# Optimization experiments

Hardware: AMD Instinct MI355X
Metric: run time of the kernel (lower is better)

Reference implementation:

```python
import jax, jax.numpy as jnp
import numpy as np

H, W, C = 768, 768, 64


def _segment_ids(mask):
    """mask: [L] int binary separator mask -> [L] int32 segment ids.
    A new grid segment starts at each rising edge (0 -> 1) of the mask;
    pixel 0 always belongs to segment 0. Equivalent to GridStructureBuilder's
    run-based row/column partition, derived via a single cumsum."""
    m = mask.astype(jnp.int32)
    prev = jnp.concatenate([jnp.zeros((1,), jnp.int32), m[:-1]])
    rising = ((m == 1) & (prev == 0)).at[0].set(False)
    return jnp.cumsum(rising.astype(jnp.int32))


def setup_inputs() -> dict:
    key = jax.random.key(0)
    k1, k2, k3 = jax.random.split(key, 3)
    return {
        "input": jax.random.normal(k1, (1, H, W, C), dtype=jnp.float32),
        "h_mask": jax.random.randint(k2, (1, H), 0, 2, dtype=jnp.int32),
        "v_mask": jax.random.randint(k3, (1, W), 0, 2, dtype=jnp.int32),
    }


def reference(input, h_mask, v_mask):
    x = input[0]                      # [H, W, C]
    h, w, c = x.shape
    row_ids = _segment_ids(h_mask[0])  # [H]
    col_ids = _segment_ids(v_mask[0])  # [W]
    # flat cell id per pixel; w is a static upper bound on the column count
    idx = (row_ids[:, None] * w + col_ids[None, :]).reshape(-1)  # [H*W]
    xf = x.reshape(h * w, c)
    n_seg = h * w                      # static upper bound on cell count
    sums = jax.ops.segment_sum(xf, idx, num_segments=n_seg)           # [n_seg, C]
    counts = jax.ops.segment_sum(jnp.ones((h * w,), x.dtype), idx,
                                 num_segments=n_seg)                  # [n_seg]
    # scatter-add of (1/area)*x == per-cell mean
    means = sums / jnp.maximum(counts, 1.0)[:, None]
    # keep_size=True: gather cell means back to every pixel
    return means[idx].reshape(1, h, w, c)
```

## Files before the change

kernel.cpp:

```cpp
#include <hip/hip_runtime.h>


#define GH 768
#define GW 768
#define GC 64
#define MAXSEG 385

enum {
    OFF_ROWSTART = 0,
    OFF_ROWEND   = OFF_ROWSTART + MAXSEG,
    OFF_COLSTART = OFF_ROWEND + MAXSEG,
    OFF_COLEND   = OFF_COLSTART + MAXSEG,
    OFF_NROWS    = OFF_COLEND + MAXSEG,
    OFF_NCOLS    = OFF_NROWS + 1,
};

__global__ __launch_bounds__(768) void seg_scan(const int* __restrict__ h_mask,
                                                const int* __restrict__ v_mask,
                                                int* __restrict__ ws) {
    __shared__ int s[GH];
    const int i = threadIdx.x;
    const bool is_row = (blockIdx.x == 0);
    const int* m = is_row ? h_mask : v_mask;

    int mi = m[i];
    int rising = 0;
    if (i > 0) rising = (mi == 1 && m[i - 1] == 0) ? 1 : 0;
    s[i] = rising;
    __syncthreads();

    for (int off = 1; off < GH; off <<= 1) {
        int add = (i >= off) ? s[i - off] : 0;
        __syncthreads();
        s[i] += add;
        __syncthreads();
    }

    const int seg  = s[i];
    const int segL = (i == 0)      ? -1 : s[i - 1];
    const int segR = (i == GH - 1) ? -2 : s[i + 1];

    int* start = ws + (is_row ? OFF_ROWSTART : OFF_COLSTART);
    int* end   = ws + (is_row ? OFF_ROWEND   : OFF_COLEND);
    if (seg != segL) start[seg] = i;
    if (seg != segR) end[seg]   = i + 1;
    if (i == GH - 1) ws[is_row ? OFF_NROWS : OFF_NCOLS] = seg + 1;
}

__global__ __launch_bounds__(256) void cell_pool(const float4* __restrict__ in,
                                                 float4* __restrict__ out,
                                                 const int* __restrict__ ws) {
    const int nrows  = ws[OFF_NROWS];
    const int ncols  = ws[OFF_NCOLS];
    const int ncells = nrows * ncols;

    const int wave   = blockIdx.x * 4 + (threadIdx.x >> 6);
    const int nwaves = gridDim.x * 4;
    const int lane   = threadIdx.x & 63;
    const int pg     = lane >> 4;
    const int cq     = lane & 15;

    for (int cell = wave; cell < ncells; cell += nwaves) {
        const int br = cell / ncols;
        const int bc = cell - br * ncols;
        const int y0 = ws[OFF_ROWSTART + br];
        const int y1 = ws[OFF_ROWEND + br];
        const int x0 = ws[OFF_COLSTART + bc];
        const int x1 = ws[OFF_COLEND + bc];

        float4 acc = make_float4(0.f, 0.f, 0.f, 0.f);
        for (int y = y0; y < y1; ++y) {
            const size_t rb = (size_t)(y * GW) * 16 + cq;
            for (int x = x0 + pg; x < x1; x += 4) {
                float4 v = in[rb + (size_t)x * 16];
                acc.x += v.x; acc.y += v.y; acc.z += v.z; acc.w += v.w;
            }
        }
        #pragma unroll
        for (int msk = 16; msk < 64; msk <<= 1) {
            acc.x += __shfl_xor(acc.x, msk, 64);
            acc.y += __shfl_xor(acc.y, msk, 64);
            acc.z += __shfl_xor(acc.z, msk, 64);
            acc.w += __shfl_xor(acc.w, msk, 64);
        }
        const float area = (float)((y1 - y0) * (x1 - x0));
        float4 mean;
        mean.x = acc.x / area; mean.y = acc.y / area;
        mean.z = acc.z / area; mean.w = acc.w / area;

        for (int y = y0; y < y1; ++y) {
            const size_t rb = (size_t)(y * GW) * 16 + cq;
            for (int x = x0 + pg; x < x1; x += 4) {
                out[rb + (size_t)x * 16] = mean;
            }
        }
    }
}

extern "C" void kernel_launch(void* const* d_in, const int* in_sizes, int n_in,
                              void* d_out, int out_size, void* d_ws, size_t ws_size,
                              hipStream_t stream) {
    const float* in  = (const float*)d_in[0];
    const int* hmask = (const int*)d_in[1];
    const int* vmask = (const int*)d_in[2];
    float* out = (float*)d_out;
    int* ws = (int*)d_ws;

    seg_scan<<<2, GH, 0, stream>>>(hmask, vmask, ws);
    cell_pool<<<2048, 256, 0, stream>>>((const float4*)in, (float4*)out, ws);
}
```

Before: 282.0 us.

## Use atomic work queue and flattened pixel loop for narrow cells

Replaces static round-robin cell assignment with a global atomic counter that hands out two cells at a time to each wave, which balances the uneven cell sizes across waves. Cells narrower than four columns now iterate over flattened pixel indices so all four pixel groups in the wave stay busy. The wide-cell loop uses two accumulators to expose more independent loads. The cost is an atomic on every dequeue, plus the queue head must be reset inside seg_scan on every launch.

```diff
diff --git a/kernel.cpp b/kernel.cpp
--- a/kernel.cpp
+++ b/kernel.cpp
@@ -3,7 +3,6 @@
 
 #define GH 768
 #define GW 768
-#define GC 64
 #define MAXSEG 385
 
 enum {
@@ -13,7 +12,12 @@
     OFF_COLEND   = OFF_COLSTART + MAXSEG,
     OFF_NROWS    = OFF_COLEND + MAXSEG,
     OFF_NCOLS    = OFF_NROWS + 1,
+    OFF_QHEAD    = OFF_NCOLS + 1,
 };
+
+__device__ __forceinline__ void acc4(float4& a, const float4 v) {
+    a.x += v.x; a.y += v.y; a.z += v.z; a.w += v.w;
+}
 
 __global__ __launch_bounds__(768) void seg_scan(const int* __restrict__ h_mask,
                                                 const int* __restrict__ v_mask,
@@ -45,53 +49,91 @@
     if (seg != segL) start[seg] = i;
     if (seg != segR) end[seg]   = i + 1;
     if (i == GH - 1) ws[is_row ? OFF_NROWS : OFF_NCOLS] = seg + 1;
+    if (i == 0 && is_row) ws[OFF_QHEAD] = 0;
 }
 
 __global__ __launch_bounds__(256) void cell_pool(const float4* __restrict__ in,
                                                  float4* __restrict__ out,
-                                                 const int* __restrict__ ws) {
+                                                 int* __restrict__ ws) {
     const int nrows  = ws[OFF_NROWS];
     const int ncols  = ws[OFF_NCOLS];
     const int ncells = nrows * ncols;
 
-    const int wave   = blockIdx.x * 4 + (threadIdx.x >> 6);
-    const int nwaves = gridDim.x * 4;
-    const int lane   = threadIdx.x & 63;
-    const int pg     = lane >> 4;
-    const int cq     = lane & 15;
+    const int lane = threadIdx.x & 63;
+    const int pg   = lane >> 4;
+    const int cq   = lane & 15;
 
-    for (int cell = wave; cell < ncells; cell += nwaves) {
-        const int br = cell / ncols;
-        const int bc = cell - br * ncols;
-        const int y0 = ws[OFF_ROWSTART + br];
-        const int y1 = ws[OFF_ROWEND + br];
-        const int x0 = ws[OFF_COLSTART + bc];
-        const int x1 = ws[OFF_COLEND + bc];
+    for (;;) {
+        int c0 = 0;
+        if (lane == 0) c0 = atomicAdd(ws + OFF_QHEAD, 2);
+        c0 = __shfl(c0, 0, 64);
+        if (c0 >= ncells) break;
+        const int cend = (c0 + 2 < ncells) ? c0 + 2 : ncells;
 
-        float4 acc = make_float4(0.f, 0.f, 0.f, 0.f);
-        for (int y = y0; y < y1; ++y) {
-            const size_t rb = (size_t)(y * GW) * 16 + cq;
-            for (int x = x0 + pg; x < x1; x += 4) {
-                float4 v = in[rb + (size_t)x * 16];
-                acc.x += v.x; acc.y += v.y; acc.z += v.z; acc.w += v.w;
+        for (int cell = c0; cell < cend; ++cell) {
+            const int br = cell / ncols;
+            const int bc = cell - br * ncols;
+            const int y0 = ws[OFF_ROWSTART + br];
+            const int y1 = ws[OFF_ROWEND + br];
+            const int x0 = ws[OFF_COLSTART + bc];
+            const int x1 = ws[OFF_COLEND + bc];
+            const int h   = y1 - y0;
+            const int wdt = x1 - x0;
+            const int npx = h * wdt;
+
+            float4 a0 = make_float4(0.f, 0.f, 0.f, 0.f);
+            float4 a1 = make_float4(0.f, 0.f, 0.f, 0.f);
+
+            if (wdt >= 4) {
+                for (int y = y0; y < y1; ++y) {
+                    const size_t rb = (size_t)(y * GW) * 16 + cq;
+                    int x = x0 + pg;
+                    for (; x + 4 < x1; x += 8) {
+                        float4 v0 = in[rb + (size_t)x * 16];
+                        float4 v1 = in[rb + (size_t)(x + 4) * 16];
+                        acc4(a0, v0);
+                        acc4(a1, v1);
+                    }
+                    for (; x < x1; x += 4) acc4(a0, in[rb + (size_t)x * 16]);
+                }
+            } else {
+                for (int base = 0; base < npx; base += 4) {
+                    const int p = base + pg;
+                    if (p < npx) {
+                        const int yy = p / wdt;
+                        const int xx = p - yy * wdt;
+                        acc4(a0, in[((size_t)((y0 + yy) * GW + x0 + xx)) * 16 + cq]);
+                    }
+                }
             }
-        }
-        #pragma unroll
-        for (int msk = 16; msk < 64; msk <<= 1) {
-            acc.x += __shfl_xor(acc.x, msk, 64);
-            acc.y += __shfl_xor(acc.y, msk, 64);
-            acc.z += __shfl_xor(acc.z, msk, 64);
-            acc.w += __shfl_xor(acc.w, msk, 64);
-        }
-        const float area = (float)((y1 - y0) * (x1 - x0));
-        float4 mean;
-        mean.x = acc.x / area; mean.y = acc.y / area;
-        mean.z = acc.z / area; mean.w = acc.w / area;
+            acc4(a0, a1);
+            #pragma unroll
+            for (int msk = 16; msk < 64; msk <<= 1) {
+                a0.x += __shfl_xor(a0.x, msk, 64);
+                a0.y += __shfl_xor(a0.y, msk, 64);
+                a0.z += __shfl_xor(a0.z, msk, 64);
+                a0.w += __shfl_xor(a0.w, msk, 64);
+            }
+            const float area = (float)npx;
+            float4 mean;
+            mean.x = a0.x / area; mean.y = a0.y / area;
+            mean.z = a0.z / area; mean.w = a0.w / area;
 
-        for (int y = y0; y < y1; ++y) {
-            const size_t rb = (size_t)(y * GW) * 16 + cq;
-            for (int x = x0 + pg; x < x1; x += 4) {
-                out[rb + (size_t)x * 16] = mean;
+            if (wdt >= 4) {
+                for (int y = y0; y < y1; ++y) {
+                    const size_t rb = (size_t)(y * GW) * 16 + cq;
+                    for (int x = x0 + pg; x < x1; x += 4)
+                        out[rb + (size_t)x * 16] = mean;
+                }
+            } else {
+                for (int base = 0; base < npx; base += 4) {
+                    const int p = base + pg;
+                    if (p < npx) {
+                        const int yy = p / wdt;
+                        const int xx = p - yy * wdt;
+                        out[((size_t)((y0 + yy) * GW + x0 + xx)) * 16 + cq] = mean;
+                    }
+                }
             }
         }
     }
```

Measured after the change: 529.0 us. +87.6%, slower.

## Split cell pooling into separable column-sum, cell-mean, and broadcast kernels

Applied to the files above, without the earlier changes.

Replaces the one-wave-per-cell pooling kernel with three kernels. The first reduces each row segment into per-column partial sums, using the output buffer as scratch. The second sums those partials over each column segment to get cell means in the workspace, and the third broadcasts the means to every pixel with fully coalesced writes. This aims to fix the poor load balance and strided small-cell access of the per-cell loop. It costs two extra launches plus the intermediate traffic, and it only runs when the workspace is large enough, otherwise falling back to the old kernel.

```diff
diff --git a/kernel.cpp b/kernel.cpp
--- a/kernel.cpp
+++ b/kernel.cpp
@@ -3,8 +3,8 @@
 
 #define GH 768
 #define GW 768
-#define GC 64
 #define MAXSEG 385
+#define ROWQ (GW * 16)
 
 enum {
     OFF_ROWSTART = 0,
@@ -13,7 +13,16 @@
     OFF_COLEND   = OFF_COLSTART + MAXSEG,
     OFF_NROWS    = OFF_COLEND + MAXSEG,
     OFF_NCOLS    = OFF_NROWS + 1,
+    OFF_RID      = OFF_NCOLS + 3,
+    OFF_CID      = OFF_RID + GH,
+    OFF_END      = OFF_CID + GW,
 };
+#define MEAN_OFF_BYTES 16384
+#define MEAN_CAP_BYTES ((size_t)MAXSEG * MAXSEG * 64 * 4)
+
+__device__ __forceinline__ void acc4(float4& a, const float4 v) {
+    a.x += v.x; a.y += v.y; a.z += v.z; a.w += v.w;
+}
 
 __global__ __launch_bounds__(768) void seg_scan(const int* __restrict__ h_mask,
                                                 const int* __restrict__ v_mask,
@@ -44,7 +53,69 @@
     int* end   = ws + (is_row ? OFF_ROWEND   : OFF_COLEND);
     if (seg != segL) start[seg] = i;
     if (seg != segR) end[seg]   = i + 1;
+    ws[(is_row ? OFF_RID : OFF_CID) + i] = seg;
     if (i == GH - 1) ws[is_row ? OFF_NROWS : OFF_NCOLS] = seg + 1;
+}
+
+__global__ __launch_bounds__(256) void col_sum(const float4* __restrict__ in,
+                                               float4* __restrict__ colsum,
+                                               const int* __restrict__ ws) {
+    const int N = ws[OFF_NROWS] * ROWQ;
+    const int stride = gridDim.x * blockDim.x;
+    for (int u = blockIdx.x * blockDim.x + threadIdx.x; u < N; u += stride) {
+        const int r   = u / ROWQ;
+        const int rem = u - r * ROWQ;
+        const int y0 = ws[OFF_ROWSTART + r];
+        const int y1 = ws[OFF_ROWEND + r];
+        float4 a0 = make_float4(0.f, 0.f, 0.f, 0.f);
+        float4 a1 = make_float4(0.f, 0.f, 0.f, 0.f);
+        int y = y0;
+        for (; y + 1 < y1; y += 2) {
+            acc4(a0, in[(size_t)y * ROWQ + rem]);
+            acc4(a1, in[(size_t)(y + 1) * ROWQ + rem]);
+        }
+        if (y < y1) acc4(a0, in[(size_t)y * ROWQ + rem]);
+        acc4(a0, a1);
+        colsum[u] = a0;
+    }
+}
+
+__global__ __launch_bounds__(256) void cell_mean(const float4* __restrict__ colsum,
+                                                 float4* __restrict__ mean,
+                                                 const int* __restrict__ ws) {
+    const int nrows = ws[OFF_NROWS];
+    const int ncols = ws[OFF_NCOLS];
+    const int N = nrows * ncols * 16;
+    const int stride = gridDim.x * blockDim.x;
+    for (int v = blockIdx.x * blockDim.x + threadIdx.x; v < N; v += stride) {
+        const int cq = v & 15;
+        const int rs = v >> 4;
+        const int r  = rs / ncols;
+        const int s  = rs - r * ncols;
+        const int x0 = ws[OFF_COLSTART + s];
+        const int x1 = ws[OFF_COLEND + s];
+        float4 a = make_float4(0.f, 0.f, 0.f, 0.f);
+        for (int x = x0; x < x1; ++x)
+            acc4(a, colsum[(size_t)r * ROWQ + x * 16 + cq]);
+        const float area =
+            (float)((ws[OFF_ROWEND + r] - ws[OFF_ROWSTART + r]) * (x1 - x0));
+        float4 mn;
+        mn.x = a.x / area; mn.y = a.y / area; mn.z = a.z / area; mn.w = a.w / area;
+        mean[v] = mn;
+    }
+}
+
+__global__ __launch_bounds__(256) void bcast(const float4* __restrict__ mean,
+                                             float4* __restrict__ out,
+                                             const int* __restrict__ ws) {
+    const int y  = blockIdx.y;
+    const int id = blockIdx.x * 256 + threadIdx.x;
+    const int x  = id >> 4;
+    const int cq = id & 15;
+    const int rid = ws[OFF_RID + y];
+    const int cid = ws[OFF_CID + x];
+    const int ncols = ws[OFF_NCOLS];
+    out[(size_t)y * ROWQ + id] = mean[((size_t)rid * ncols + cid) * 16 + cq];
 }
 
 __global__ __launch_bounds__(256) void cell_pool(const float4* __restrict__ in,
@@ -68,31 +139,26 @@
         const int x0 = ws[OFF_COLSTART + bc];
         const int x1 = ws[OFF_COLEND + bc];
 
-        float4 acc = make_float4(0.f, 0.f, 0.f, 0.f);
+        float4 a = make_float4(0.f, 0.f, 0.f, 0.f);
         for (int y = y0; y < y1; ++y) {
-            const size_t rb = (size_t)(y * GW) * 16 + cq;
-            for (int x = x0 + pg; x < x1; x += 4) {
-                float4 v = in[rb + (size_t)x * 16];
-                acc.x += v.x; acc.y += v.y; acc.z += v.z; acc.w += v.w;
-            }
+            const size_t rb = (size_t)y * ROWQ + cq;
+            for (int x = x0 + pg; x < x1; x += 4)
+                acc4(a, in[rb + (size_t)x * 16]);
         }
         #pragma unroll
         for (int msk = 16; msk < 64; msk <<= 1) {
-            acc.x += __shfl_xor(acc.x, msk, 64);
-            acc.y += __shfl_xor(acc.y, msk, 64);
-            acc.z += __shfl_xor(acc.z, msk, 64);
-            acc.w += __shfl_xor(acc.w, msk, 64);
+            a.x += __shfl_xor(a.x, msk, 64);
+            a.y += __shfl_xor(a.y, msk, 64);
+            a.z += __shfl_xor(a.z, msk, 64);
+            a.w += __shfl_xor(a.w, msk, 64);
         }
         const float area = (float)((y1 - y0) * (x1 - x0));
-        float4 mean;
-        mean.x = acc.x / area; mean.y = acc.y / area;
-        mean.z = acc.z / area; mean.w = acc.w / area;
-
+        float4 mn;
+        mn.x = a.x / area; mn.y = a.y / area; mn.z = a.z / area; mn.w = a.w / area;
         for (int y = y0; y < y1; ++y) {
-            const size_t rb = (size_t)(y * GW) * 16 + cq;
-            for (int x = x0 + pg; x < x1; x += 4) {
-                out[rb + (size_t)x * 16] = mean;
-            }
+            const size_t rb = (size_t)y * ROWQ + cq;
+            for (int x = x0 + pg; x < x1; x += 4)
+                out[rb + (size_t)x * 16] = mn;
         }
     }
 }
@@ -107,5 +173,15 @@
     int* ws = (int*)d_ws;
 
     seg_scan<<<2, GH, 0, stream>>>(hmask, vmask, ws);
-    cell_pool<<<2048, 256, 0, stream>>>((const float4*)in, (float4*)out, ws);
+
+    if (ws_size >= MEAN_OFF_BYTES + MEAN_CAP_BYTES) {
+        float4* colsum = (float4*)d_out;
+        float4* mean   = (float4*)((char*)d_ws + MEAN_OFF_BYTES);
+        col_sum<<<4096, 256, 0, stream>>>((const float4*)in, colsum, ws);
+        cell_mean<<<2048, 256, 0, stream>>>(colsum, mean, ws);
+        dim3 cgrid(GW * 16 / 256, GH);
+        bcast<<<cgrid, 256, 0, stream>>>(mean, (float4*)out, ws);
+    } else {
+        cell_pool<<<2048, 256, 0, stream>>>((const float4*)in, (float4*)out, ws);
+    }
 }
```

Measured after the change: 291.1 us. 1.03x slower.

## Pool cells via row-strip column tiles with shared-memory column sums

Applied to the files above, without the earlier changes.

Adds a strip_pool kernel in which each block handles one row segment across a tile of up to 64 columns built from whole column segments. Column sums go to shared memory and per-cell means are derived from them, so loads and stores are wide and coalesced instead of one wave walking tiny cells. The scan kernel now packs column segments into tiles and sets a fallback flag that sends wide segments or too many tiles back to the old cell_pool path. The cost is an extra launch, a serial single-thread tiling loop, and blocks that exit early.

```diff
diff --git a/kernel.cpp b/kernel.cpp
--- a/kernel.cpp
+++ b/kernel.cpp
@@ -3,8 +3,10 @@
 
 #define GH 768
 #define GW 768
-#define GC 64
 #define MAXSEG 385
+#define ROWQ (GW * 16)
+#define TILEW 64
+#define MAXT 26
 
 enum {
     OFF_ROWSTART = 0,
@@ -12,20 +14,31 @@
     OFF_COLSTART = OFF_ROWEND + MAXSEG,
     OFF_COLEND   = OFF_COLSTART + MAXSEG,
     OFF_NROWS    = OFF_COLEND + MAXSEG,
-    OFF_NCOLS    = OFF_NROWS + 1,
+    OFF_NCOLS,
+    OFF_NTILES,
+    OFF_FB,
+    OFF_CID,
+    OFF_TX0 = OFF_CID + GW,
+    OFF_TX1 = OFF_TX0 + MAXT,
+    OFF_TFS = OFF_TX1 + MAXT,
+    OFF_END = OFF_TFS + MAXT,
 };
+
+__device__ __forceinline__ void acc4(float4& a, const float4 v) {
+    a.x += v.x; a.y += v.y; a.z += v.z; a.w += v.w;
+}
 
 __global__ __launch_bounds__(768) void seg_scan(const int* __restrict__ h_mask,
                                                 const int* __restrict__ v_mask,
                                                 int* __restrict__ ws) {
     __shared__ int s[GH];
+    __shared__ int lstart[MAXSEG], lend[MAXSEG];
     const int i = threadIdx.x;
     const bool is_row = (blockIdx.x == 0);
     const int* m = is_row ? h_mask : v_mask;
 
-    int mi = m[i];
     int rising = 0;
-    if (i > 0) rising = (mi == 1 && m[i - 1] == 0) ? 1 : 0;
+    if (i > 0) rising = (m[i] == 1 && m[i - 1] == 0) ? 1 : 0;
     s[i] = rising;
     __syncthreads();
 
@@ -42,14 +55,107 @@
 
     int* start = ws + (is_row ? OFF_ROWSTART : OFF_COLSTART);
     int* end   = ws + (is_row ? OFF_ROWEND   : OFF_COLEND);
-    if (seg != segL) start[seg] = i;
-    if (seg != segR) end[seg]   = i + 1;
+    if (seg != segL) { start[seg] = i;     if (!is_row) lstart[seg] = i; }
+    if (seg != segR) { end[seg]   = i + 1; if (!is_row) lend[seg] = i + 1; }
     if (i == GH - 1) ws[is_row ? OFF_NROWS : OFF_NCOLS] = seg + 1;
+
+    if (!is_row) {
+        ws[OFF_CID + i] = seg;
+        __syncthreads();
+        if (i == 0) {
+            const int nseg = s[GH - 1] + 1;
+            int fb = 0, t = 0, first = 0, curw = 0;
+            for (int sg = 0; sg < nseg; ++sg) {
+                const int w = lend[sg] - lstart[sg];
+                if (w > TILEW) fb = 1;
+                if (curw > 0 && curw + w > TILEW) {
+                    if (t < MAXT) {
+                        ws[OFF_TX0 + t] = lstart[first];
+                        ws[OFF_TX1 + t] = lend[sg - 1];
+                        ws[OFF_TFS + t] = first;
+                    }
+                    ++t; first = sg; curw = 0;
+                }
+                curw += w;
+            }
+            if (t < MAXT) {
+                ws[OFF_TX0 + t] = lstart[first];
+                ws[OFF_TX1 + t] = lend[nseg - 1];
+                ws[OFF_TFS + t] = first;
+            }
+            ++t;
+            if (t > MAXT) fb = 1;
+            ws[OFF_NTILES] = (t <= MAXT) ? t : 0;
+            ws[OFF_FB] = fb;
+        }
+    }
+}
+
+__global__ __launch_bounds__(256) void strip_pool(const float4* __restrict__ in,
+                                                  float4* __restrict__ out,
+                                                  const int* __restrict__ ws) {
+    if (ws[OFF_FB]) return;
+    const int r = blockIdx.y;
+    const int t = blockIdx.x;
+    if (r >= ws[OFF_NROWS] || t >= ws[OFF_NTILES]) return;
+
+    const int y0  = ws[OFF_ROWSTART + r];
+    const int y1  = ws[OFF_ROWEND + r];
+    const int tx0 = ws[OFF_TX0 + t];
+    const int tx1 = ws[OFF_TX1 + t];
+    const int tfs = ws[OFF_TFS + t];
+    const int nu  = (tx1 - tx0) * 16;
+    const int tid = threadIdx.x;
+    const int u0 = tid, u1 = tid + 256, u2 = tid + 512, u3 = tid + 768;
+
+    float4 a0 = make_float4(0.f,0.f,0.f,0.f), a1 = a0, a2 = a0, a3 = a0;
+    for (int y = y0; y < y1; ++y) {
+        const float4* rp = in + (size_t)y * ROWQ + (size_t)tx0 * 16;
+        if (u0 < nu) acc4(a0, rp[u0]);
+        if (u1 < nu) acc4(a1, rp[u1]);
+        if (u2 < nu) acc4(a2, rp[u2]);
+        if (u3 < nu) acc4(a3, rp[u3]);
+    }
+
+    __shared__ float4 colsum[TILEW * 16];
+    __shared__ float4 means[TILEW * 16];
+    if (u0 < nu) colsum[u0] = a0;
+    if (u1 < nu) colsum[u1] = a1;
+    if (u2 < nu) colsum[u2] = a2;
+    if (u3 < nu) colsum[u3] = a3;
+    __syncthreads();
+
+    const int nst = ws[OFF_CID + tx1 - 1] - tfs + 1;
+    const float hh = (float)(y1 - y0);
+    for (int v = tid; v < nst * 16; v += 256) {
+        const int sl = v >> 4, cq = v & 15;
+        const int gx0 = ws[OFF_COLSTART + tfs + sl] - tx0;
+        const int gx1 = ws[OFF_COLEND + tfs + sl] - tx0;
+        float4 a = make_float4(0.f,0.f,0.f,0.f);
+        for (int x = gx0; x < gx1; ++x) acc4(a, colsum[x * 16 + cq]);
+        const float area = hh * (float)(gx1 - gx0);
+        means[v] = make_float4(a.x / area, a.y / area, a.z / area, a.w / area);
+    }
+    __syncthreads();
+
+    float4 m0, m1, m2, m3;
+    if (u0 < nu) m0 = means[(ws[OFF_CID + tx0 + (u0 >> 4)] - tfs) * 16 + (u0 & 15)];
+    if (u1 < nu) m1 = means[(ws[OFF_CID + tx0 + (u1 >> 4)] - tfs) * 16 + (u1 & 15)];
+    if (u2 < nu) m2 = means[(ws[OFF_CID + tx0 + (u2 >> 4)] - tfs) * 16 + (u2 & 15)];
+    if (u3 < nu) m3 = means[(ws[OFF_CID + tx0 + (u3 >> 4)] - tfs) * 16 + (u3 & 15)];
+    for (int y = y0; y < y1; ++y) {
+        float4* op = out + (size_t)y * ROWQ + (size_t)tx0 * 16;
+        if (u0 < nu) op[u0] = m0;
+        if (u1 < nu) op[u1] = m1;
+        if (u2 < nu) op[u2] = m2;
+        if (u3 < nu) op[u3] = m3;
+    }
 }
 
 __global__ __launch_bounds__(256) void cell_pool(const float4* __restrict__ in,
                                                  float4* __restrict__ out,
                                                  const int* __restrict__ ws) {
+    if (ws[OFF_FB] == 0) return;
     const int nrows  = ws[OFF_NROWS];
     const int ncols  = ws[OFF_NCOLS];
     const int ncells = nrows * ncols;
@@ -68,31 +174,25 @@
         const int x0 = ws[OFF_COLSTART + bc];
         const int x1 = ws[OFF_COLEND + bc];
 
-        float4 acc = make_float4(0.f, 0.f, 0.f, 0.f);
+        float4 a = make_float4(0.f,0.f,0.f,0.f);
         for (int y = y0; y < y1; ++y) {
-            const size_t rb = (size_t)(y * GW) * 16 + cq;
-            for (int x = x0 + pg; x < x1; x += 4) {
-                float4 v = in[rb + (size_t)x * 16];
-                acc.x += v.x; acc.y += v.y; acc.z += v.z; acc.w += v.w;
-            }
+            const size_t rb = (size_t)y * ROWQ + cq;
+            for (int x = x0 + pg; x < x1; x += 4)
+                acc4(a, in[rb + (size_t)x * 16]);
         }
         #pragma unroll
         for (int msk = 16; msk < 64; msk <<= 1) {
-            acc.x += __shfl_xor(acc.x, msk, 64);
-            acc.y += __shfl_xor(acc.y, msk, 64);
-            acc.z += __shfl_xor(acc.z, msk, 64);
-            acc.w += __shfl_xor(acc.w, msk, 64);
+            a.x += __shfl_xor(a.x, msk, 64);
+            a.y += __shfl_xor(a.y, msk, 64);
+            a.z += __shfl_xor(a.z, msk, 64);
+            a.w += __shfl_xor(a.w, msk, 64);
         }
         const float area = (float)((y1 - y0) * (x1 - x0));
-        float4 mean;
-        mean.x = acc.x / area; mean.y = acc.y / area;
-        mean.z = acc.z / area; mean.w = acc.w / area;
-
+        float4 mn = make_float4(a.x / area, a.y / area, a.z / area, a.w / area);
         for (int y = y0; y < y1; ++y) {
-            const size_t rb = (size_t)(y * GW) * 16 + cq;
-            for (int x = x0 + pg; x < x1; x += 4) {
-                out[rb + (size_t)x * 16] = mean;
-            }
+            const size_t rb = (size_t)y * ROWQ + cq;
+            for (int x = x0 + pg; x < x1; x += 4)
+                out[rb + (size_t)x * 16] = mn;
         }
     }
 }
@@ -107,5 +207,7 @@
     int* ws = (int*)d_ws;
 
     seg_scan<<<2, GH, 0, stream>>>(hmask, vmask, ws);
+    dim3 grid(MAXT, MAXSEG);
+    strip_pool<<<grid, 256, 0, stream>>>((const float4*)in, (float4*)out, ws);
     cell_pool<<<2048, 256, 0, stream>>>((const float4*)in, (float4*)out, ws);
 }
```

Result: slower. 297.9 us (+5.6%).
